# Optimization experiments

Measured on AMD Instinct MI355X. Metric: run time of the kernel, lower is better.

Reference implementation:

```python
import jax, jax.numpy as jnp
import numpy as np

ALPHA = 32.0 ** 2
MASK_VALUE = -jnp.finfo(jnp.float32).max


def rotate_half(t):
    d = t.shape[-1] // 2
    x1, x2 = t[..., :d], t[..., d:]
    return jnp.concatenate([-x2, x1], axis=-1)


def apply_rotary_pos_emb(freqs, t):
    # freqs: [n, rot_dim], t: [b, h, n, d]
    rot_dim = freqs.shape[-1]
    t_rot, t_pass = t[..., :rot_dim], t[..., rot_dim:]
    t_rot = t_rot * jnp.cos(freqs) + rotate_half(t_rot) * jnp.sin(freqs)
    return jnp.concatenate([t_rot, t_pass], axis=-1)


def stable_softmax(t, alpha=ALPHA):
    t = t / alpha
    t = t - jax.lax.stop_gradient(jnp.max(t, axis=-1, keepdims=True))
    return jax.nn.softmax(t * alpha, axis=-1)


def setup_inputs() -> dict:
    key = jax.random.key(0)
    ks = jax.random.split(key, 8)
    b, n, dim = 2, 2048, 1024
    h, dh = 16, 64
    inner = h * dh
    rot_dim = 32
    return {
        "x": jax.random.normal(ks[0], (b, n, dim), jnp.float32),
        "mask": jnp.ones((b, n), dtype=bool),
        "rotary_pos_emb": jax.random.normal(ks[1], (n, rot_dim), jnp.float32),
        "null_k": jax.random.normal(ks[2], (h, 1, dh), jnp.float32),
        "null_v": jax.random.normal(ks[3], (h, 1, dh), jnp.float32),
        "th_w": jax.random.normal(ks[4], (h, h), jnp.float32) * (1.0 / h),
        "w_q": jax.random.normal(ks[5], (dim, inner), jnp.float32) * (dim ** -0.5),
        "w_kv": jax.random.normal(ks[6], (dim, 2 * inner), jnp.float32) * (dim ** -0.5),
        "w_out": jax.random.normal(ks[7], (inner, dim), jnp.float32) * (inner ** -0.5),
        "b_out": jnp.zeros((dim,), jnp.float32),
    }


def reference(x, mask, rotary_pos_emb, null_k, null_v, th_w, w_q, w_kv, w_out, b_out):
    b, n, _ = x.shape
    h, _, dh = null_k.shape
    scale = dh ** -0.5

    q = x @ w_q                      # [b, n, h*dh]
    kv = x @ w_kv                    # [b, n, 2*h*dh]
    k, v = jnp.split(kv, 2, axis=-1)

    def to_heads(t):
        return t.reshape(b, n, h, dh).transpose(0, 2, 1, 3)  # [b, h, n, d]

    q, k, v = map(to_heads, (q, k, v))

    # rotary applied to q, k AND v (as in source)
    q = apply_rotary_pos_emb(rotary_pos_emb, q)
    k = apply_rotary_pos_emb(rotary_pos_emb, k)
    v = apply_rotary_pos_emb(rotary_pos_emb, v)

    # prepend learned null key/value token
    nk = jnp.broadcast_to(null_k[None], (b, h, 1, dh))
    nv = jnp.broadcast_to(null_v[None], (b, h, 1, dh))
    k = jnp.concatenate([nk, k], axis=2)  # [b, h, n+1, d]
    v = jnp.concatenate([nv, v], axis=2)

    q = q * scale
    sim = jnp.einsum('bhid,bhjd->bhij', q, k)  # [b, h, n, n+1]

    # key padding mask (null token always visible)
    key_mask = jnp.pad(mask, ((0, 0), (1, 0)), constant_values=True)
    sim = jnp.where(key_mask[:, None, None, :], sim, MASK_VALUE)

    # causal mask: padded col > row + (j - i)
    i, j = sim.shape[-2], sim.shape[-1]
    causal = jnp.arange(j)[None, :] > jnp.arange(i)[:, None] + (j - i)
    sim = jnp.where(causal, MASK_VALUE, sim)

    attn = stable_softmax(sim)
    # talking heads: 1x1 conv over head channel == head mixing matrix
    attn = jnp.einsum('gh,bhij->bgij', th_w, attn)

    out = jnp.einsum('bhij,bhjd->bhid', attn, v)
    out = out.transpose(0, 2, 1, 3).reshape(b, n, h * dh)
    return out @ w_out + b_out
```

## Files before the change

### kernel.cpp

```cpp
#include <hip/hip_runtime.h>
#include <hip/hip_bf16.h>
#include <cstdint>
#include <cstddef>

using bf16 = __hip_bfloat16;
typedef __attribute__((ext_vector_type(8))) short short8;
typedef __attribute__((ext_vector_type(4))) short short4v;
typedef __attribute__((ext_vector_type(4))) float f32x4;

constexpr int BB  = 2;
constexpr int SEQ = 2048;
constexpr int NH  = 16;
constexpr int HD  = 64;
constexpr int KPAD = 2112;
constexpr int DM  = 1024;

static __device__ __forceinline__ bf16 f2b(float v) { return __float2bfloat16(v); }
static __device__ __forceinline__ float b2f(bf16 v) { return __bfloat162float(v); }

static __device__ __forceinline__ void gload16(const bf16* g, bf16* l) {
  __builtin_amdgcn_global_load_lds(
      (const __attribute__((address_space(1))) void*)g,
      (__attribute__((address_space(3))) void*)l, 16, 0, 0);
}

__global__ __launch_bounds__(256) void cast_x_kernel(const float* __restrict__ src,
                                                     bf16* __restrict__ dst, int n4) {
  int idx = blockIdx.x * 256 + threadIdx.x;
  if (idx >= n4) return;
  float4 v = *(const float4*)(src + (size_t)idx * 4);
  bf16 o[4] = {f2b(v.x), f2b(v.y), f2b(v.z), f2b(v.w)};
  *(short4v*)(dst + (size_t)idx * 4) = *(short4v*)o;
}

__global__ __launch_bounds__(256) void zero_kernel(float* __restrict__ dst, int n4) {
  int idx = blockIdx.x * 256 + threadIdx.x;
  if (idx >= n4) return;
  float4 z; z.x = 0.f; z.y = 0.f; z.z = 0.f; z.w = 0.f;
  *(float4*)(dst + (size_t)idx * 4) = z;
}

__global__ __launch_bounds__(256) void cast_o_kernel(const float* __restrict__ src,
                                                     bf16* __restrict__ dst, int n4) {
  int idx = blockIdx.x * 256 + threadIdx.x;
  if (idx >= n4) return;
  float4 v = *(const float4*)(src + (size_t)idx * 4);
  bf16 o[4] = {f2b(v.x), f2b(v.y), f2b(v.z), f2b(v.w)};
  *(short4v*)(dst + (size_t)idx * 4) = *(short4v*)o;
}

__global__ __launch_bounds__(256) void transpose_cast_kernel(const float* __restrict__ src,
                                                             bf16* __restrict__ dst,
                                                             int colsN, int ldDst) {
  int n0 = blockIdx.x * 32, k0 = blockIdx.y * 32;
  __shared__ alignas(16) float t[32][33];
  int tid = threadIdx.x;
  {
    int r = tid >> 3, c4 = (tid & 7) * 4;
    float4 v = *(const float4*)(src + (size_t)(k0 + r) * colsN + n0 + c4);
    t[r][c4 + 0] = v.x; t[r][c4 + 1] = v.y; t[r][c4 + 2] = v.z; t[r][c4 + 3] = v.w;
  }
  __syncthreads();
  {
    int nl = tid >> 3, k4 = (tid & 7) * 4;
    bf16 o[4];
#pragma unroll
    for (int u = 0; u < 4; ++u) o[u] = f2b(t[k4 + u][nl]);
    *(short4v*)(dst + (size_t)(n0 + nl) * ldDst + k0 + k4) = *(short4v*)o;
  }
}

template <bool OUT_BF16, bool BIAS>
__global__ __launch_bounds__(256) void gemm_lds_kernel(
    const bf16* __restrict__ A, int lda,
    const bf16* __restrict__ BT, int ldb,
    void* __restrict__ Cv, int ldc,
    const float* __restrict__ bias, int K) {
  constexpr int BK = 32;
  const int tid = threadIdx.x, wave = tid >> 6, lane = tid & 63;
  const int lr = lane & 15, lq = lane >> 4;
  const int wm = wave >> 1, wn = wave & 1;
  const int m0 = blockIdx.y * 128, n0 = blockIdx.x * 128;
  const int srow = lane >> 2;
  const int scol = (lane & 3) * 8;

  __shared__ alignas(16) bf16 ash[128 * BK];
  __shared__ alignas(16) bf16 bsh[128 * BK];

  f32x4 acc[4][4];
#pragma unroll
  for (int i = 0; i < 4; ++i)
#pragma unroll
    for (int j = 0; j < 4; ++j)
#pragma unroll
      for (int r = 0; r < 4; ++r) acc[i][j][r] = 0.f;

  const int nk = K / BK;
  for (int kt = 0; kt < nk; ++kt) {
    const int k0 = kt * BK;
#pragma unroll
    for (int c = 0; c < 2; ++c) {
      const int rbase = wave * 32 + c * 16;
      gload16(A + (size_t)(m0 + rbase + srow) * lda + k0 + scol, ash + rbase * BK);
      gload16(BT + (size_t)(n0 + rbase + srow) * ldb + k0 + scol, bsh + rbase * BK);
    }
    __syncthreads();
    short8 af[4], bfv[4];
#pragma unroll
    for (int i = 0; i < 4; ++i)
      af[i] = *(const short8*)&ash[(wm * 64 + i * 16 + lr) * BK + lq * 8];
#pragma unroll
    for (int j = 0; j < 4; ++j)
      bfv[j] = *(const short8*)&bsh[(wn * 64 + j * 16 + lr) * BK + lq * 8];
#pragma unroll
    for (int i = 0; i < 4; ++i)
#pragma unroll
      for (int j = 0; j < 4; ++j)
        acc[i][j] = __builtin_amdgcn_mfma_f32_16x16x32_bf16(af[i], bfv[j], acc[i][j], 0, 0, 0);
    __syncthreads();
  }
#pragma unroll
  for (int i = 0; i < 4; ++i) {
    int row0 = m0 + wm * 64 + i * 16 + lq * 4;
#pragma unroll
    for (int j = 0; j < 4; ++j) {
      int col = n0 + wn * 64 + j * 16 + lr;
      float bv = BIAS ? bias[col] : 0.f;
#pragma unroll
      for (int r = 0; r < 4; ++r) {
        float v = acc[i][j][r] + bv;
        if (OUT_BF16) ((bf16*)Cv)[(size_t)(row0 + r) * ldc + col] = f2b(v);
        else          ((float*)Cv)[(size_t)(row0 + r) * ldc + col] = v;
      }
    }
  }
}

__global__ __launch_bounds__(256) void rope_build_kernel(
    const bf16* __restrict__ qkv, const float* __restrict__ rot,
    const float* __restrict__ nullk, const float* __restrict__ nullv,
    bf16* __restrict__ Q, bf16* __restrict__ Kt, bf16* __restrict__ Vt) {
  const int blk = blockIdx.x;
  const int ic = blk & 63;
  const int h = (blk >> 6) & 15;
  const int b = blk >> 10;
  const int i0 = ic * 32;
  const int tid = threadIdx.x;
  const int bh = b * NH + h;

  __shared__ alignas(16) bf16 sh[33][192];
  __shared__ alignas(16) float cs[33][32], sn[33][32];

  for (int c = 0; c < 4; ++c) {
    int idx = tid + c * 256;
    if (idx < 33 * 24) {
      int row = idx / 24, ch = idx % 24;
      int p = ch >> 3, cc = (ch & 7) * 8;
      int i = i0 - 1 + row;
      if (i >= 0)
        *(short8*)&sh[row][p * 64 + cc] =
            *(const short8*)(qkv + (size_t)(b * SEQ + i) * 3072 + p * 1024 + h * 64 + cc);
    }
  }
  for (int c = 0; c < 5; ++c) {
    int idx = tid + c * 256;
    if (idx < 33 * 32) {
      int row = idx >> 5, d = idx & 31;
      int i = i0 - 1 + row;
      if (i >= 0) {
        float f = rot[i * 32 + d];
        cs[row][d] = cosf(f);
        sn[row][d] = sinf(f);
      }
    }
  }
  __syncthreads();

  auto ropev = [&](int row, int off, int d) -> float {
    float v = b2f(sh[row][off + d]);
    if (d < 32) {
      float c = cs[row][d], s = sn[row][d];
      float v2 = b2f(sh[row][off + (d < 16 ? d + 16 : d - 16)]);
      return d < 16 ? v * c - v2 * s : v * c + v2 * s;
    }
    return v;
  };

  const int dA = tid & 63;
#pragma unroll
  for (int rep = 0; rep < 8; ++rep) {
    int il = rep * 4 + (tid >> 6);
    int row = il + 1;
    int i = i0 + il;
    float qv = ropev(row, 0, dA) * 0.125f;
    float kv = ropev(row, 64, dA);
    Q[((size_t)bh * SEQ + i) * HD + dA] = f2b(qv);
    Kt[((size_t)bh * KPAD + (i + 1)) * HD + dA] = f2b(kv);
  }
  {
    int d = tid >> 2;
    int g0 = (tid & 3) * 8;
    bf16 tmp[8];
#pragma unroll
    for (int u = 0; u < 8; ++u) {
      int j = i0 + g0 + u;
      if (j == 0) tmp[u] = f2b(nullv[h * 64 + d]);
      else        tmp[u] = f2b(ropev(j - i0, 128, d));
    }
    *(short8*)(Vt + ((size_t)bh * HD + d) * KPAD + i0 + g0) = *(short8*)tmp;
  }
  if (i0 == 0 && tid < 64)
    Kt[(size_t)bh * KPAD * HD + tid] = f2b(nullk[h * 64 + tid]);
  if (ic == 63 && tid < 64)
    Vt[((size_t)bh * HD + tid) * KPAD + 2048] = f2b(ropev(32, 128, tid));
}

__global__ __launch_bounds__(256) void denom_kernel(
    const bf16* __restrict__ Q, const bf16* __restrict__ Kt, float* __restrict__ Linv) {
  const int bh = blockIdx.x;
  const int i0 = blockIdx.y * 32;
  const int tid = threadIdx.x;
  const int wave = tid >> 6, lane = tid & 63;
  const int lr = lane & 15, lq = lane >> 4;
  const bf16* Qp = Q + (size_t)bh * SEQ * HD;
  const bf16* Kp = Kt + (size_t)bh * KPAD * HD;

  short8 af[2][2];
#pragma unroll
  for (int fi = 0; fi < 2; ++fi)
#pragma unroll
    for (int ks = 0; ks < 2; ++ks)
      af[fi][ks] = *(const short8*)(Qp + (size_t)(i0 + fi * 16 + lr) * HD + ks * 32 + lq * 8);

  const int tmax = (i0 + 32) >> 6;
  float lacc[2][4];
#pragma unroll
  for (int fi = 0; fi < 2; ++fi)
#pragma unroll
    for (int r = 0; r < 4; ++r) lacc[fi][r] = 0.f;

  for (int t = wave; t <= tmax; t += 4) {
    f32x4 s[2][4];
#pragma unroll
    for (int fi = 0; fi < 2; ++fi)
#pragma unroll
      for (int fj = 0; fj < 4; ++fj)
#pragma unroll
        for (int r = 0; r < 4; ++r) s[fi][fj][r] = 0.f;
#pragma unroll
    for (int fj = 0; fj < 4; ++fj) {
      const bf16* kp = Kp + (size_t)(t * 64 + fj * 16 + lr) * HD + lq * 8;
      short8 b0 = *(const short8*)kp;
      short8 b1 = *(const short8*)(kp + 32);
#pragma unroll
      for (int fi = 0; fi < 2; ++fi) {
        s[fi][fj] = __builtin_amdgcn_mfma_f32_16x16x32_bf16(af[fi][0], b0, s[fi][fj], 0, 0, 0);
        s[fi][fj] = __builtin_amdgcn_mfma_f32_16x16x32_bf16(af[fi][1], b1, s[fi][fj], 0, 0, 0);
      }
    }
#pragma unroll
    for (int fi = 0; fi < 2; ++fi)
#pragma unroll
      for (int fj = 0; fj < 4; ++fj)
#pragma unroll
        for (int r = 0; r < 4; ++r) {
          int i = i0 + fi * 16 + lq * 4 + r;
          int j = t * 64 + fj * 16 + lr;
          if (j <= i + 1) lacc[fi][r] += __expf(s[fi][fj][r]);
        }
  }
#pragma unroll
  for (int m = 1; m <= 8; m <<= 1)
#pragma unroll
    for (int fi = 0; fi < 2; ++fi)
#pragma unroll
      for (int r = 0; r < 4; ++r) lacc[fi][r] += __shfl_xor(lacc[fi][r], m, 64);

  __shared__ alignas(16) float lsh[4][32];
  if (lr == 0) {
#pragma unroll
    for (int fi = 0; fi < 2; ++fi)
#pragma unroll
      for (int r = 0; r < 4; ++r) lsh[wave][fi * 16 + lq * 4 + r] = lacc[fi][r];
  }
  __syncthreads();
  if (tid < 32)
    Linv[(size_t)bh * SEQ + i0 + tid] =
        1.f / (lsh[0][tid] + lsh[1][tid] + lsh[2][tid] + lsh[3][tid]);
}

__global__ __launch_bounds__(512) void pmix_kernel(
    const bf16* __restrict__ Q, const bf16* __restrict__ Kt,
    const float* __restrict__ Linv, const float* __restrict__ thw,
    bf16* __restrict__ Pm) {
  const int t = blockIdx.x;
  const int ic = blockIdx.y;
  const int i0 = ic * 32;
  const int tid = threadIdx.x, wave = tid >> 6, lane = tid & 63;
  const int lr = lane & 15, lq = lane >> 4;
  const int tmax = (i0 + 32) >> 6;

  short8 zero8;
#pragma unroll
  for (int e = 0; e < 8; ++e) zero8[e] = 0;

  if (t > tmax) {
    if (t > (ic >> 1) + 1) return;
#pragma unroll
    for (int k = 0; k < 8; ++k) {
      int idx = tid + k * 512;
      int g = idx >> 8, rest = idx & 255;
      int il = rest >> 3, jc = (rest & 7) * 8;
      *(short8*)(Pm + ((size_t)g * SEQ + i0 + il) * KPAD + t * 64 + jc) = zero8;
    }
    return;
  }

  __shared__ alignas(16) bf16 p_sh[2048][16];
  __shared__ alignas(16) bf16 p2c[16][512];

  f32x4 fzero;
#pragma unroll
  for (int r = 0; r < 4; ++r) fzero[r] = 0.f;

  short8 wfrag = zero8;
  if (lq < 2) {
    bf16 tmp[8];
#pragma unroll
    for (int e = 0; e < 8; ++e) tmp[e] = f2b(thw[lr * 16 + lq * 8 + e]);
    wfrag = *(short8*)tmp;
  }

#pragma unroll
  for (int hh = 0; hh < 2; ++hh) {
    const int h = wave * 2 + hh;
    const bf16* Qp = Q + ((size_t)h * SEQ + i0) * HD;
    const bf16* Kp = Kt + ((size_t)h * KPAD + t * 64) * HD;
    short8 qf[2][2];
#pragma unroll
    for (int fi = 0; fi < 2; ++fi)
#pragma unroll
      for (int ks = 0; ks < 2; ++ks)
        qf[fi][ks] = *(const short8*)(Qp + (size_t)(fi * 16 + lr) * HD + ks * 32 + lq * 8);
    float linv[2][4];
#pragma unroll
    for (int fi = 0; fi < 2; ++fi)
#pragma unroll
      for (int r = 0; r < 4; ++r)
        linv[fi][r] = Linv[(size_t)h * SEQ + i0 + fi * 16 + lq * 4 + r];

    f32x4 s[2][4];
#pragma unroll
    for (int fi = 0; fi < 2; ++fi)
#pragma unroll
      for (int fj = 0; fj < 4; ++fj) s[fi][fj] = fzero;
#pragma unroll
    for (int fj = 0; fj < 4; ++fj) {
      const bf16* kp = Kp + (size_t)(fj * 16 + lr) * HD + lq * 8;
      short8 b0 = *(const short8*)kp;
      short8 b1 = *(const short8*)(kp + 32);
#pragma unroll
      for (int fi = 0; fi < 2; ++fi) {
        s[fi][fj] = __builtin_amdgcn_mfma_f32_16x16x32_bf16(qf[fi][0], b0, s[fi][fj], 0, 0, 0);
        s[fi][fj] = __builtin_amdgcn_mfma_f32_16x16x32_bf16(qf[fi][1], b1, s[fi][fj], 0, 0, 0);
      }
    }
#pragma unroll
    for (int fi = 0; fi < 2; ++fi)
#pragma unroll
      for (int fj = 0; fj < 4; ++fj)
#pragma unroll
        for (int r = 0; r < 4; ++r) {
          int il = fi * 16 + lq * 4 + r;
          int jl = fj * 16 + lr;
          int i = i0 + il, j = t * 64 + jl;
          float p = (j <= i + 1) ? __expf(s[fi][fj][r]) * linv[fi][r] : 0.f;
          p_sh[il * 64 + jl][h] = f2b(p);
        }
  }
  __syncthreads();

  for (int ch = 0; ch < 4; ++ch) {
#pragma unroll
    for (int q = 0; q < 4; ++q) {
      const int cl = (wave * 4 + q) * 16 + lr;
      const int c  = ch * 512 + cl;
      short8 bfrag = zero8;
      if (lq < 2) bfrag = *(const short8*)&p_sh[c][lq * 8];
      f32x4 d = __builtin_amdgcn_mfma_f32_16x16x32_bf16(wfrag, bfrag, fzero, 0, 0, 0);
      const int es = cl ^ (((cl >> 6) & 7) << 3);
#pragma unroll
      for (int r = 0; r < 4; ++r)
        p2c[lq * 4 + r][es] = f2b(d[r]);
    }
    __syncthreads();
#pragma unroll
    for (int it = 0; it < 2; ++it) {
      const int u = tid + it * 512;
      const int g = u >> 6, rest = u & 63;
      const int il = rest >> 3, jc = (rest & 7) * 8;
      const int es = (il * 64 + jc) ^ (il << 3);
      short8 v = *(const short8*)&p2c[g][es];
      *(short8*)(Pm + ((size_t)g * SEQ + i0 + ch * 8 + il) * KPAD + t * 64 + jc) = v;
    }
    __syncthreads();
  }
}

__global__ __launch_bounds__(256) void pv64_kernel(
    const bf16* __restrict__ Pm, const bf16* __restrict__ Vt, bf16* __restrict__ oh) {
  const int g = blockIdx.x;
  const int m0 = blockIdx.y * 64;
  const int tid = threadIdx.x, w = tid >> 6, lane = tid & 63;
  const int lr = lane & 15, lq = lane >> 4;
  const bf16* A  = Pm + (size_t)g * SEQ * KPAD;
  const bf16* BT = Vt + (size_t)g * HD * KPAD;

  __shared__ alignas(16) bf16 ash[64][40];
  __shared__ alignas(16) bf16 bsh[64][40];

  f32x4 acc[4];
#pragma unroll
  for (int j = 0; j < 4; ++j)
#pragma unroll
    for (int r = 0; r < 4; ++r) acc[j][r] = 0.f;

  const int nk = m0 / 32 + 3;
  for (int kt = 0; kt < nk; ++kt) {
    const int k0 = kt * 32;
    *(short8*)&ash[tid >> 2][(tid & 3) * 8] =
        *(const short8*)(A + (size_t)(m0 + (tid >> 2)) * KPAD + k0 + (tid & 3) * 8);
    *(short8*)&bsh[tid >> 2][(tid & 3) * 8] =
        *(const short8*)(BT + (size_t)(tid >> 2) * KPAD + k0 + (tid & 3) * 8);
    __syncthreads();
    short8 af = *(const short8*)&ash[w * 16 + lr][lq * 8];
#pragma unroll
    for (int j = 0; j < 4; ++j) {
      short8 bfv = *(const short8*)&bsh[j * 16 + lr][lq * 8];
      acc[j] = __builtin_amdgcn_mfma_f32_16x16x32_bf16(af, bfv, acc[j], 0, 0, 0);
    }
    __syncthreads();
  }
#pragma unroll
  for (int j = 0; j < 4; ++j)
#pragma unroll
    for (int r = 0; r < 4; ++r)
      oh[(size_t)(m0 + w * 16 + lq * 4 + r) * DM + g * 64 + j * 16 + lr] = f2b(acc[j][r]);
}

__global__ __launch_bounds__(512) void fused2_kernel(
    const bf16* __restrict__ Q, const bf16* __restrict__ Kt, const bf16* __restrict__ Vt,
    const float* __restrict__ Linv, const float* __restrict__ thw,
    float* __restrict__ ohf) {
  const int pairIdx = blockIdx.x >> 2;
  const int b  = (blockIdx.x >> 1) & 1;
  const int jh = blockIdx.x & 1;
  const int tid = threadIdx.x;
  const int w = tid >> 6, lane = tid & 63;
  const int lr = lane & 15, lq = lane >> 4;

  __shared__ alignas(16) bf16 p_sh[1024 * 24];
  __shared__ alignas(16) bf16 p2[16 * 1032];

  short8 zero8;
#pragma unroll
  for (int e = 0; e < 8; ++e) zero8[e] = 0;
  f32x4 fzero;
#pragma unroll
  for (int r = 0; r < 4; ++r) fzero[r] = 0.f;

  short8 wfrag = zero8;
  if (lq < 2) {
    bf16 tmp[8];
#pragma unroll
    for (int e = 0; e < 8; ++e) tmp[e] = f2b(thw[lr * 16 + lq * 8 + e]);
    wfrag = *(short8*)tmp;
  }

#pragma unroll
  for (int sel = 0; sel < 2; ++sel) {
    const int ic = sel ? 127 - pairIdx : pairIdx;
    const int i0 = ic * 16;
    const int n = ((i0 + 16) >> 6) + 1;
    const int half = (n + 1) >> 1;
    const int t0 = jh ? half : 0;
    const int t1 = jh ? n : half;

    short8 qf[2][2];
    float linv[2][4];
    const bf16* Vp[2];
    const bf16* Kp[2];
#pragma unroll
    for (int hh = 0; hh < 2; ++hh) {
      const int h = w + hh * 8;
      const int bh = b * NH + h;
      const bf16* Qp = Q + ((size_t)bh * SEQ + i0) * HD;
#pragma unroll
      for (int ks = 0; ks < 2; ++ks)
        qf[hh][ks] = *(const short8*)(Qp + (size_t)lr * HD + ks * 32 + lq * 8);
#pragma unroll
      for (int r = 0; r < 4; ++r)
        linv[hh][r] = Linv[(size_t)bh * SEQ + i0 + lq * 4 + r];
      Kp[hh] = Kt + (size_t)bh * KPAD * HD;
      Vp[hh] = Vt + (size_t)bh * HD * KPAD;
    }

    f32x4 oacc[2][4];
#pragma unroll
    for (int hh = 0; hh < 2; ++hh)
#pragma unroll
      for (int fn = 0; fn < 4; ++fn) oacc[hh][fn] = fzero;

    for (int t = t0; t < t1; ++t) {
#pragma unroll
      for (int hh = 0; hh < 2; ++hh) {
        const int h = w + hh * 8;
        f32x4 s[4];
#pragma unroll
        for (int fj = 0; fj < 4; ++fj) s[fj] = fzero;
#pragma unroll
        for (int fj = 0; fj < 4; ++fj) {
          const bf16* kp = Kp[hh] + (size_t)(t * 64 + fj * 16 + lr) * HD + lq * 8;
          short8 b0 = *(const short8*)kp;
          short8 b1 = *(const short8*)(kp + 32);
          s[fj] = __builtin_amdgcn_mfma_f32_16x16x32_bf16(qf[hh][0], b0, s[fj], 0, 0, 0);
          s[fj] = __builtin_amdgcn_mfma_f32_16x16x32_bf16(qf[hh][1], b1, s[fj], 0, 0, 0);
        }
#pragma unroll
        for (int fj = 0; fj < 4; ++fj)
#pragma unroll
          for (int r = 0; r < 4; ++r) {
            int il = lq * 4 + r;
            int jl = fj * 16 + lr;
            int i = i0 + il, j = t * 64 + jl;
            float p = (j <= i + 1) ? __expf(s[fj][r]) * linv[hh][r] : 0.f;
            p_sh[(il * 64 + jl) * 24 + h] = f2b(p);
          }
      }
      __syncthreads();
#pragma unroll
      for (int q = 0; q < 8; ++q) {
        const int c = (w * 8 + q) * 16 + lr;
        short8 bfrag = zero8;
        if (lq < 2) bfrag = *(const short8*)&p_sh[c * 24 + lq * 8];
        f32x4 d = __builtin_amdgcn_mfma_f32_16x16x32_bf16(wfrag, bfrag, fzero, 0, 0, 0);
        const int sc = c ^ (((c >> 6) & 7) << 3);
#pragma unroll
        for (int r = 0; r < 4; ++r)
          p2[(lq * 4 + r) * 1032 + sc] = f2b(d[r]);
      }
      __syncthreads();
#pragma unroll
      for (int hh = 0; hh < 2; ++hh) {
        const int h = w + hh * 8;
        short8 pa[2];
#pragma unroll
        for (int ks = 0; ks < 2; ++ks) {
          const int c = lr * 64 + ks * 32 + lq * 8;
          const int sc = c ^ (((c >> 6) & 7) << 3);
          pa[ks] = *(const short8*)&p2[h * 1032 + sc];
        }
#pragma unroll
        for (int fn = 0; fn < 4; ++fn) {
          const bf16* vp = Vp[hh] + (size_t)(fn * 16 + lr) * KPAD + t * 64 + lq * 8;
          short8 v0 = *(const short8*)vp;
          short8 v1 = *(const short8*)(vp + 32);
          oacc[hh][fn] = __builtin_amdgcn_mfma_f32_16x16x32_bf16(pa[0], v0, oacc[hh][fn], 0, 0, 0);
          oacc[hh][fn] = __builtin_amdgcn_mfma_f32_16x16x32_bf16(pa[1], v1, oacc[hh][fn], 0, 0, 0);
        }
      }
    }
#pragma unroll
    for (int hh = 0; hh < 2; ++hh) {
      const int h = w + hh * 8;
#pragma unroll
      for (int fn = 0; fn < 4; ++fn)
#pragma unroll
        for (int r = 0; r < 4; ++r)
          atomicAdd(ohf + (size_t)(b * SEQ + i0 + lq * 4 + r) * DM + h * 64 + fn * 16 + lr,
                    oacc[hh][fn][r]);
    }
    __syncthreads();
  }
}

extern "C" void kernel_launch(void* const* d_in, const int* in_sizes, int n_in,
                              void* d_out, int out_size, void* d_ws, size_t ws_size,
                              hipStream_t stream) {
  const float* x     = (const float*)d_in[0];
  const float* rot   = (const float*)d_in[2];
  const float* nullk = (const float*)d_in[3];
  const float* nullv = (const float*)d_in[4];
  const float* thw   = (const float*)d_in[5];
  const float* wq    = (const float*)d_in[6];
  const float* wkv   = (const float*)d_in[7];
  const float* wout  = (const float*)d_in[8];
  const float* bout  = (const float*)d_in[9];
  float* out = (float*)d_out;

  char* ws = (char*)d_ws;
  size_t off = 0;
  auto alloc = [&](size_t bytes) { char* p = ws + off; off += (bytes + 255) & ~(size_t)255; return p; };
  bf16* x_bf    = (bf16*)alloc((size_t)BB * SEQ * DM * 2);
  bf16* wqkv_t  = (bf16*)alloc((size_t)3072 * 1024 * 2);
  bf16* wout_t  = (bf16*)alloc((size_t)1024 * 1024 * 2);
  bf16* Qb      = (bf16*)alloc((size_t)BB * NH * SEQ * HD * 2);
  bf16* Kt      = (bf16*)alloc((size_t)BB * NH * KPAD * HD * 2);
  bf16* Vt      = (bf16*)alloc((size_t)BB * NH * HD * KPAD * 2);
  float* Linv   = (float*)alloc((size_t)BB * NH * SEQ * 4);
  bf16* oh      = (bf16*)alloc((size_t)BB * SEQ * DM * 2);
  const size_t shared_off = off;
  bf16* qkv_bf = (bf16*)(ws + shared_off);
  bf16* Pm     = (bf16*)(ws + shared_off);
  const size_t PM_BYTES = (size_t)NH * SEQ * KPAD * 2;
  const bool pathA = (shared_off + PM_BYTES) <= ws_size;
  float* ohf = (float*)qkv_bf;

  cast_x_kernel<<<(BB * SEQ * DM / 4 + 255) / 256, 256, 0, stream>>>(x, x_bf, BB * SEQ * DM / 4);
  transpose_cast_kernel<<<dim3(1024 / 32, 1024 / 32), 256, 0, stream>>>(wq, wqkv_t, 1024, 1024);
  transpose_cast_kernel<<<dim3(2048 / 32, 1024 / 32), 256, 0, stream>>>(wkv, wqkv_t + (size_t)1024 * 1024, 2048, 1024);
  transpose_cast_kernel<<<dim3(1024 / 32, 1024 / 32), 256, 0, stream>>>(wout, wout_t, 1024, 1024);

  gemm_lds_kernel<true, false>
      <<<dim3(3072 / 128, 4096 / 128), 256, 0, stream>>>(
          x_bf, 1024, wqkv_t, 1024, qkv_bf, 3072, nullptr, 1024);

  rope_build_kernel<<<BB * NH * (SEQ / 32), 256, 0, stream>>>(qkv_bf, rot, nullk, nullv, Qb, Kt, Vt);

  denom_kernel<<<dim3(BB * NH, SEQ / 32), 256, 0, stream>>>(Qb, Kt, Linv);

  if (pathA) {
    for (int b = 0; b < BB; ++b) {
      pmix_kernel<<<dim3(33, 64), 512, 0, stream>>>(
          Qb + (size_t)b * NH * SEQ * HD,
          Kt + (size_t)b * NH * KPAD * HD,
          Linv + (size_t)b * NH * SEQ, thw, Pm);
      pv64_kernel<<<dim3(16, 32), 256, 0, stream>>>(
          Pm, Vt + (size_t)b * NH * HD * KPAD, oh + (size_t)b * SEQ * DM);
    }
  } else {
    zero_kernel<<<(BB * SEQ * DM / 4 + 255) / 256, 256, 0, stream>>>(ohf, BB * SEQ * DM / 4);
    fused2_kernel<<<256, 512, 0, stream>>>(Qb, Kt, Vt, Linv, thw, ohf);
    cast_o_kernel<<<(BB * SEQ * DM / 4 + 255) / 256, 256, 0, stream>>>(ohf, oh, BB * SEQ * DM / 4);
  }

  gemm_lds_kernel<false, true>
      <<<dim3(1024 / 128, 4096 / 128), 256, 0, stream>>>(
          oh, 1024, wout_t, 1024, out, 1024, bout, 1024);
}
```

Baseline: 379.9 us.

## Restructure pmix kernel into two row halves with padded LDS and swapped grid

The pmix kernel now works on its 32 query rows in two 16-row halves. K fragments for both heads are loaded once into registers and reused across the halves, and the per-head probability staging buffer is halved in size with a padded stride of 20 to cut LDS bank conflicts. The grid axes are swapped so that consecutive blocks share the same key tile t, which may improve L2 reuse of K. In exchange the kernel keeps more K fragments live in registers and adds extra __syncthreads between halves.

```diff
diff --git a/kernel.cpp b/kernel.cpp
--- a/kernel.cpp
+++ b/kernel.cpp
@@ -17,6 +17,9 @@
 
 static __device__ __forceinline__ bf16 f2b(float v) { return __float2bfloat16(v); }
 static __device__ __forceinline__ float b2f(bf16 v) { return __bfloat162float(v); }
+static __device__ __forceinline__ uint16_t f2u(float v) {
+  union { bf16 b; uint16_t u; } c; c.b = __float2bfloat16(v); return c.u;
+}
 
 static __device__ __forceinline__ void gload16(const bf16* g, bf16* l) {
   __builtin_amdgcn_global_load_lds(
@@ -293,8 +296,8 @@
     const bf16* __restrict__ Q, const bf16* __restrict__ Kt,
     const float* __restrict__ Linv, const float* __restrict__ thw,
     bf16* __restrict__ Pm) {
-  const int t = blockIdx.x;
-  const int ic = blockIdx.y;
+  const int ic = blockIdx.x;
+  const int t  = blockIdx.y;
   const int i0 = ic * 32;
   const int tid = threadIdx.x, wave = tid >> 6, lane = tid & 63;
   const int lr = lane & 15, lq = lane >> 4;
@@ -316,7 +319,8 @@
     return;
   }
 
-  __shared__ alignas(16) bf16 p_sh[2048][16];
+  constexpr int PST = 20;
+  __shared__ alignas(16) bf16 p_sh[1024 * PST];
   __shared__ alignas(16) bf16 p2c[16][512];
 
   f32x4 fzero;
@@ -331,79 +335,90 @@
     wfrag = *(short8*)tmp;
   }
 
+  short8 kf[2][4][2];
 #pragma unroll
   for (int hh = 0; hh < 2; ++hh) {
     const int h = wave * 2 + hh;
-    const bf16* Qp = Q + ((size_t)h * SEQ + i0) * HD;
     const bf16* Kp = Kt + ((size_t)h * KPAD + t * 64) * HD;
-    short8 qf[2][2];
-#pragma unroll
-    for (int fi = 0; fi < 2; ++fi)
-#pragma unroll
-      for (int ks = 0; ks < 2; ++ks)
-        qf[fi][ks] = *(const short8*)(Qp + (size_t)(fi * 16 + lr) * HD + ks * 32 + lq * 8);
-    float linv[2][4];
-#pragma unroll
-    for (int fi = 0; fi < 2; ++fi)
-#pragma unroll
-      for (int r = 0; r < 4; ++r)
-        linv[fi][r] = Linv[(size_t)h * SEQ + i0 + fi * 16 + lq * 4 + r];
-
-    f32x4 s[2][4];
-#pragma unroll
-    for (int fi = 0; fi < 2; ++fi)
-#pragma unroll
-      for (int fj = 0; fj < 4; ++fj) s[fi][fj] = fzero;
 #pragma unroll
     for (int fj = 0; fj < 4; ++fj) {
       const bf16* kp = Kp + (size_t)(fj * 16 + lr) * HD + lq * 8;
-      short8 b0 = *(const short8*)kp;
-      short8 b1 = *(const short8*)(kp + 32);
-#pragma unroll
-      for (int fi = 0; fi < 2; ++fi) {
-        s[fi][fj] = __builtin_amdgcn_mfma_f32_16x16x32_bf16(qf[fi][0], b0, s[fi][fj], 0, 0, 0);
-        s[fi][fj] = __builtin_amdgcn_mfma_f32_16x16x32_bf16(qf[fi][1], b1, s[fi][fj], 0, 0, 0);
-      }
-    }
-#pragma unroll
-    for (int fi = 0; fi < 2; ++fi)
-#pragma unroll
-      for (int fj = 0; fj < 4; ++fj)
-#pragma unroll
-        for (int r = 0; r < 4; ++r) {
-          int il = fi * 16 + lq * 4 + r;
-          int jl = fj * 16 + lr;
-          int i = i0 + il, j = t * 64 + jl;
-          float p = (j <= i + 1) ? __expf(s[fi][fj][r]) * linv[fi][r] : 0.f;
-          p_sh[il * 64 + jl][h] = f2b(p);
-        }
-  }
-  __syncthreads();
-
-  for (int ch = 0; ch < 4; ++ch) {
-#pragma unroll
-    for (int q = 0; q < 4; ++q) {
-      const int cl = (wave * 4 + q) * 16 + lr;
-      const int c  = ch * 512 + cl;
-      short8 bfrag = zero8;
-      if (lq < 2) bfrag = *(const short8*)&p_sh[c][lq * 8];
-      f32x4 d = __builtin_amdgcn_mfma_f32_16x16x32_bf16(wfrag, bfrag, fzero, 0, 0, 0);
-      const int es = cl ^ (((cl >> 6) & 7) << 3);
+      kf[hh][fj][0] = *(const short8*)kp;
+      kf[hh][fj][1] = *(const short8*)(kp + 32);
+    }
+  }
+
+#pragma unroll
+  for (int half = 0; half < 2; ++half) {
+    const int ib = i0 + half * 16;
+#pragma unroll
+    for (int hh = 0; hh < 2; ++hh) {
+      const int h = wave * 2 + hh;
+      const bf16* Qp = Q + ((size_t)h * SEQ + ib) * HD;
+      short8 qf0 = *(const short8*)(Qp + (size_t)lr * HD + lq * 8);
+      short8 qf1 = *(const short8*)(Qp + (size_t)lr * HD + 32 + lq * 8);
+      float linv[4];
 #pragma unroll
       for (int r = 0; r < 4; ++r)
-        p2c[lq * 4 + r][es] = f2b(d[r]);
+        linv[r] = Linv[(size_t)h * SEQ + ib + lq * 4 + r];
+
+      f32x4 s[4];
+#pragma unroll
+      for (int fj = 0; fj < 4; ++fj) {
+        s[fj] = fzero;
+        s[fj] = __builtin_amdgcn_mfma_f32_16x16x32_bf16(qf0, kf[hh][fj][0], s[fj], 0, 0, 0);
+        s[fj] = __builtin_amdgcn_mfma_f32_16x16x32_bf16(qf1, kf[hh][fj][1], s[fj], 0, 0, 0);
+      }
+      if (hh == 0) {
+#pragma unroll
+        for (int fj = 0; fj < 4; ++fj)
+#pragma unroll
+          for (int r = 0; r < 4; ++r) {
+            int il = lq * 4 + r, jl = fj * 16 + lr;
+            int i = ib + il, j = t * 64 + jl;
+            float p = (j <= i + 1) ? __expf(s[fj][r]) * linv[r] : 0.f;
+            ((uint16_t*)p_sh)[(il * 64 + jl) * PST + wave * 2] = f2u(p);
+          }
+      } else {
+#pragma unroll
+        for (int fj = 0; fj < 4; ++fj)
+#pragma unroll
+          for (int r = 0; r < 4; ++r) {
+            int il = lq * 4 + r, jl = fj * 16 + lr;
+            int i = ib + il, j = t * 64 + jl;
+            float p = (j <= i + 1) ? __expf(s[fj][r]) * linv[r] : 0.f;
+            ((uint16_t*)p_sh)[(il * 64 + jl) * PST + wave * 2 + 1] = f2u(p);
+          }
+      }
     }
     __syncthreads();
-#pragma unroll
-    for (int it = 0; it < 2; ++it) {
-      const int u = tid + it * 512;
-      const int g = u >> 6, rest = u & 63;
-      const int il = rest >> 3, jc = (rest & 7) * 8;
-      const int es = (il * 64 + jc) ^ (il << 3);
-      short8 v = *(const short8*)&p2c[g][es];
-      *(short8*)(Pm + ((size_t)g * SEQ + i0 + ch * 8 + il) * KPAD + t * 64 + jc) = v;
-    }
-    __syncthreads();
+
+#pragma unroll
+    for (int ch = 0; ch < 2; ++ch) {
+#pragma unroll
+      for (int q = 0; q < 4; ++q) {
+        const int cl = (wave * 4 + q) * 16 + lr;
+        const int c  = ch * 512 + cl;
+        short8 bfrag = zero8;
+        if (lq < 2) bfrag = *(const short8*)&p_sh[c * PST + lq * 8];
+        f32x4 d = __builtin_amdgcn_mfma_f32_16x16x32_bf16(wfrag, bfrag, fzero, 0, 0, 0);
+        const int es = cl ^ (((cl >> 6) & 7) << 3);
+#pragma unroll
+        for (int r = 0; r < 4; ++r)
+          p2c[lq * 4 + r][es] = f2b(d[r]);
+      }
+      __syncthreads();
+#pragma unroll
+      for (int it = 0; it < 2; ++it) {
+        const int u = tid + it * 512;
+        const int g = u >> 6, rest = u & 63;
+        const int il = rest >> 3, jc = (rest & 7) * 8;
+        const int es = (il * 64 + jc) ^ (il << 3);
+        short8 v = *(const short8*)&p2c[g][es];
+        *(short8*)(Pm + ((size_t)g * SEQ + ib + ch * 8 + il) * KPAD + t * 64 + jc) = v;
+      }
+      __syncthreads();
+    }
   }
 }
 
@@ -631,7 +646,7 @@
 
   if (pathA) {
     for (int b = 0; b < BB; ++b) {
-      pmix_kernel<<<dim3(33, 64), 512, 0, stream>>>(
+      pmix_kernel<<<dim3(64, 33), 512, 0, stream>>>(
           Qb + (size_t)b * NH * SEQ * HD,
           Kt + (size_t)b * NH * KPAD * HD,
           Linv + (size_t)b * NH * SEQ, thw, Pm);
```

New measurement: 430.6 us. 13.3% more time.
